# Kernel tuning notes

Hardware: AMD Instinct MI355X
Metric: run time of the kernel (lower is better)

## Reference

```python
import jax, jax.numpy as jnp
import numpy as np

N_NODES = 100000
N_EDGES = 1600000
IN_F = 512
OUT_F = 128


def setup_inputs() -> dict:
    key = jax.random.key(0)
    k1, k2, k3, k4, k5 = jax.random.split(key, 5)
    x = jax.random.normal(k1, (N_NODES, IN_F), dtype=jnp.float32)
    adj_row = jnp.sort(jax.random.randint(k2, (N_EDGES,), 0, N_NODES, dtype=jnp.int32))
    adj_col = jax.random.randint(k3, (N_EDGES,), 0, N_NODES, dtype=jnp.int32)
    adj_vals = jax.random.uniform(k4, (N_EDGES,), dtype=jnp.float32)
    # Xavier-uniform init like nn.init.xavier_uniform_
    limit = float(np.sqrt(6.0 / (IN_F + OUT_F)))
    weight = jax.random.uniform(k5, (IN_F, OUT_F), minval=-limit, maxval=limit, dtype=jnp.float32)
    return {"x": x, "adj_row": adj_row, "adj_col": adj_col, "adj_vals": adj_vals, "weight": weight}


def reference(x, adj_row, adj_col, adj_vals, weight):
    # support = input @ weight  (dense GEMM; torch.spmm with dense-equivalent input)
    support = x @ weight                      # [N, OUT_F]
    # output = adj @ support, adj in COO: gather cols, scale, segment-sum by row
    msgs = adj_vals[:, None] * support[adj_col]          # [E, OUT_F]
    output = jax.ops.segment_sum(msgs, adj_row, num_segments=N_NODES)  # [N, OUT_F]
    return output
```

## Files before the change

kernel.cpp:

```cpp
#include <hip/hip_runtime.h>
#include <hip/hip_bf16.h>

typedef __bf16 bf16;
typedef __attribute__((ext_vector_type(8))) __bf16 bf16x8;
typedef __attribute__((ext_vector_type(4))) __bf16 bf16x4;
typedef __attribute__((ext_vector_type(2))) __bf16 bf16x2;
typedef __attribute__((ext_vector_type(4))) float f32x4;

#define IN_F 512
#define OUT_F 128
#define BM 64
#define BK 64
#define NKT (IN_F / BK)
#define CHUNK 128
#define UNR 16

__global__ __launch_bounds__(256) void wt_convert_kernel(const float* __restrict__ w,
                                                         bf16* __restrict__ wt_frag) {
    int o = blockIdx.x * 256 + threadIdx.x;
    int e   = o & 7;
    int l   = (o >> 3) & 63;
    int nb  = (o >> 9) & 7;
    int kkt = o >> 12;
    int n = nb * 16 + (l & 15);
    int k = (kkt >> 1) * 64 + (kkt & 1) * 32 + (l >> 4) * 8 + e;
    wt_frag[o] = (bf16)w[k * OUT_F + n];
}

__global__ __launch_bounds__(256) void gemm_kernel(const float* __restrict__ x,
                                                   const bf16* __restrict__ wt_frag,
                                                   bf16* __restrict__ support,
                                                   float* __restrict__ out,
                                                   int n_nodes) {
    __shared__ bf16 As[2][BM * BK];

    const int tid  = threadIdx.x;
    const int lane = tid & 63;
    const int wid  = tid >> 6;
    const int row0 = blockIdx.x * BM;

    float4 av[4];

    auto load_tile = [&](int kt) {
        const int k0 = kt * BK;
        #pragma unroll
        for (int i = 0; i < 4; ++i) {
            int li = i * 256 + tid;
            int r = li >> 4, c4 = li & 15;
            int grow = row0 + r;
            float4 v = {0.f, 0.f, 0.f, 0.f};
            if (grow < n_nodes)
                v = *reinterpret_cast<const float4*>(x + (size_t)grow * IN_F + k0 + c4 * 4);
            av[i] = v;
        }
    };

    auto write_tile = [&](int buf) {
        char* Ab = (char*)As[buf];
        #pragma unroll
        for (int i = 0; i < 4; ++i) {
            int li = i * 256 + tid;
            int r = li >> 4, c4 = li & 15;
            bf16x4 b;
            b[0] = (bf16)av[i].x; b[1] = (bf16)av[i].y;
            b[2] = (bf16)av[i].z; b[3] = (bf16)av[i].w;
            *reinterpret_cast<bf16x4*>(Ab + ((r * 128 + c4 * 8) ^ ((r & 7) << 4))) = b;
        }
    };

    load_tile(0);

    {
        float4 z = {0.f, 0.f, 0.f, 0.f};
        const size_t lim = (size_t)n_nodes * OUT_F;
        #pragma unroll
        for (int i = 0; i < 8; ++i) {
            size_t off = (size_t)row0 * OUT_F + (size_t)(i * 256 + tid) * 4;
            if (off < lim)
                *reinterpret_cast<float4*>(out + off) = z;
        }
    }

    write_tile(0);
    __syncthreads();

    f32x4 acc[4][2] = {};

    for (int kt = 0; kt < NKT; ++kt) {
        const int cur = kt & 1;

        bf16x8 b[2][2];
        #pragma unroll
        for (int kk = 0; kk < 2; ++kk)
            #pragma unroll
            for (int n = 0; n < 2; ++n) {
                int f = (kt * 2 + kk) * 8 + (wid * 2 + n);
                b[kk][n] = *reinterpret_cast<const bf16x8*>(wt_frag + ((size_t)f * 64 + lane) * 8);
            }

        if (kt < NKT - 1) load_tile(kt + 1);

        const char* Ab = (const char*)As[cur];
        #pragma unroll
        for (int kk = 0; kk < 2; ++kk) {
            const int kbyte = kk * 64 + (lane >> 4) * 16;
            bf16x8 a[4];
            #pragma unroll
            for (int m = 0; m < 4; ++m) {
                int r = m * 16 + (lane & 15);
                a[m] = *reinterpret_cast<const bf16x8*>(Ab + ((r * 128 + kbyte) ^ ((r & 7) << 4)));
            }
            #pragma unroll
            for (int m = 0; m < 4; ++m)
                #pragma unroll
                for (int n = 0; n < 2; ++n)
                    acc[m][n] = __builtin_amdgcn_mfma_f32_16x16x32_bf16(a[m], b[kk][n], acc[m][n], 0, 0, 0);
        }

        if (kt < NKT - 1) {
            write_tile(cur ^ 1);
            __syncthreads();
        }
    }

    #pragma unroll
    for (int m = 0; m < 4; ++m) {
        #pragma unroll
        for (int n = 0; n < 2; ++n) {
            #pragma unroll
            for (int j = 0; j < 4; ++j) {
                int gm = row0 + m * 16 + (lane >> 4) * 4 + j;
                int gn = wid * 32 + n * 16 + (lane & 15);
                if (gm < n_nodes)
                    support[(size_t)gm * OUT_F + gn] = (bf16)acc[m][n][j];
            }
        }
    }
}

__global__ __launch_bounds__(64) void scatter_kernel(const int* __restrict__ adj_row,
                                                     const int* __restrict__ adj_col,
                                                     const float* __restrict__ adj_vals,
                                                     const bf16* __restrict__ support,
                                                     float* __restrict__ out,
                                                     int n_edges) {
    __shared__ int   srow[CHUNK];
    __shared__ int   scol[CHUNK];
    __shared__ float sval[CHUNK];

    const int t  = threadIdx.x;
    const int e0 = blockIdx.x * CHUNK;
    const int nE = min(CHUNK, n_edges - e0);

    for (int i = t; i < CHUNK; i += 64) {
        if (i < nE) {
            srow[i] = adj_row[e0 + i];
            scol[i] = adj_col[e0 + i];
            sval[i] = adj_vals[e0 + i];
        } else {
            srow[i] = adj_row[e0 + nE - 1];
            scol[i] = 0;
            sval[i] = 0.f;
        }
    }
    __syncthreads();

    const int firstRow = srow[0];

    float accx = 0.f, accy = 0.f;
    int   cur = firstRow;

    for (int i0 = 0; i0 < CHUNK; i0 += UNR) {
        float mx[UNR], my[UNR];
        #pragma unroll
        for (int u = 0; u < UNR; ++u) {
            int   c = scol[i0 + u];
            float s = sval[i0 + u];
            bf16x2 v = *reinterpret_cast<const bf16x2*>(support + (size_t)c * OUT_F + t * 2);
            mx[u] = s * (float)v[0];
            my[u] = s * (float)v[1];
        }
        #pragma unroll
        for (int u = 0; u < UNR; ++u) {
            int r = srow[i0 + u];
            if (r != cur) {
                float* dst = out + (size_t)cur * OUT_F + t * 2;
                if (cur == firstRow) {
                    atomicAdd(dst, accx); atomicAdd(dst + 1, accy);
                } else {
                    dst[0] = accx; dst[1] = accy;
                }
                accx = 0.f; accy = 0.f;
                cur = r;
            }
            accx += mx[u]; accy += my[u];
        }
    }
    float* dst = out + (size_t)cur * OUT_F + t * 2;
    atomicAdd(dst, accx); atomicAdd(dst + 1, accy);
}

extern "C" void kernel_launch(void* const* d_in, const int* in_sizes, int n_in,
                              void* d_out, int out_size, void* d_ws, size_t ws_size,
                              hipStream_t stream) {
    const float* x        = (const float*)d_in[0];
    const int*   adj_row  = (const int*)d_in[1];
    const int*   adj_col  = (const int*)d_in[2];
    const float* adj_vals = (const float*)d_in[3];
    const float* weight   = (const float*)d_in[4];
    float*       out      = (float*)d_out;

    const int n_nodes = in_sizes[0] / IN_F;
    const int n_edges = in_sizes[1];

    bf16* support = (bf16*)d_ws;
    bf16* wt_frag = (bf16*)((char*)d_ws + (size_t)n_nodes * OUT_F * 2);

    wt_convert_kernel<<<(IN_F * OUT_F) / 256, 256, 0, stream>>>(weight, wt_frag);

    int gemm_blocks = (n_nodes + BM - 1) / BM;
    gemm_kernel<<<gemm_blocks, 256, 0, stream>>>(x, wt_frag, support, out, n_nodes);

    int scat_blocks = (n_edges + CHUNK - 1) / CHUNK;
    scatter_kernel<<<scat_blocks, 64, 0, stream>>>(adj_row, adj_col, adj_vals,
                                                   support, out, n_edges);
}
```

Measured before the change: 126.3 us.

## Stage GEMM input tiles with direct global-to-LDS loads, converting to bf16 at read

The GEMM kernel now copies fp32 x tiles straight into shared memory with global_load_lds DMA, using an XOR-swizzled chunk layout. This replaces the old path that loaded into registers, converted to bf16 and wrote to LDS. The bf16 conversion now happens when A fragments are read from LDS before the MFMAs. The aim is to cut register pressure and VALU/LDS-write work in the load path and let loads overlap compute better. In exchange, LDS use doubles, every read converts fp32, and LDS read traffic per fragment doubles.

```diff
diff --git a/kernel.cpp b/kernel.cpp
--- a/kernel.cpp
+++ b/kernel.cpp
@@ -14,6 +14,12 @@
 #define NKT (IN_F / BK)
 #define CHUNK 128
 #define UNR 16
+
+__device__ __forceinline__ void gload_lds16(const void* g, void* l) {
+    __builtin_amdgcn_global_load_lds(
+        (const __attribute__((address_space(1))) void*)g,
+        (__attribute__((address_space(3))) void*)l, 16, 0, 0);
+}
 
 __global__ __launch_bounds__(256) void wt_convert_kernel(const float* __restrict__ w,
                                                          bf16* __restrict__ wt_frag) {
@@ -32,43 +38,29 @@
                                                    bf16* __restrict__ support,
                                                    float* __restrict__ out,
                                                    int n_nodes) {
-    __shared__ bf16 As[2][BM * BK];
+    __shared__ float As[2][BM * BK];
 
     const int tid  = threadIdx.x;
     const int lane = tid & 63;
     const int wid  = tid >> 6;
     const int row0 = blockIdx.x * BM;
 
-    float4 av[4];
-
-    auto load_tile = [&](int kt) {
+    auto stage_tile = [&](int kt, int buf) {
         const int k0 = kt * BK;
         #pragma unroll
         for (int i = 0; i < 4; ++i) {
-            int li = i * 256 + tid;
-            int r = li >> 4, c4 = li & 15;
+            int li  = i * 256 + tid;
+            int r   = li >> 4;
+            int c16 = li & 15;
             int grow = row0 + r;
-            float4 v = {0.f, 0.f, 0.f, 0.f};
-            if (grow < n_nodes)
-                v = *reinterpret_cast<const float4*>(x + (size_t)grow * IN_F + k0 + c4 * 4);
-            av[i] = v;
+            if (grow >= n_nodes) grow = n_nodes - 1;
+            const float* g = x + (size_t)grow * IN_F + k0 + ((c16 ^ (r & 7)) << 2);
+            float* l = &As[buf][(size_t)(i * 256 + (tid & ~63)) * 4];
+            gload_lds16(g, l);
         }
     };
 
-    auto write_tile = [&](int buf) {
-        char* Ab = (char*)As[buf];
-        #pragma unroll
-        for (int i = 0; i < 4; ++i) {
-            int li = i * 256 + tid;
-            int r = li >> 4, c4 = li & 15;
-            bf16x4 b;
-            b[0] = (bf16)av[i].x; b[1] = (bf16)av[i].y;
-            b[2] = (bf16)av[i].z; b[3] = (bf16)av[i].w;
-            *reinterpret_cast<bf16x4*>(Ab + ((r * 128 + c4 * 8) ^ ((r & 7) << 4))) = b;
-        }
-    };
-
-    load_tile(0);
+    stage_tile(0, 0);
 
     {
         float4 z = {0.f, 0.f, 0.f, 0.f};
@@ -80,8 +72,6 @@
                 *reinterpret_cast<float4*>(out + off) = z;
         }
     }
-
-    write_tile(0);
     __syncthreads();
 
     f32x4 acc[4][2] = {};
@@ -98,17 +88,22 @@
                 b[kk][n] = *reinterpret_cast<const bf16x8*>(wt_frag + ((size_t)f * 64 + lane) * 8);
             }
 
-        if (kt < NKT - 1) load_tile(kt + 1);
-
-        const char* Ab = (const char*)As[cur];
+        if (kt < NKT - 1) stage_tile(kt + 1, cur ^ 1);
+
+        const float* Af = As[cur];
         #pragma unroll
         for (int kk = 0; kk < 2; ++kk) {
-            const int kbyte = kk * 64 + (lane >> 4) * 16;
             bf16x8 a[4];
             #pragma unroll
             for (int m = 0; m < 4; ++m) {
-                int r = m * 16 + (lane & 15);
-                a[m] = *reinterpret_cast<const bf16x8*>(Ab + ((r * 128 + kbyte) ^ ((r & 7) << 4)));
+                int r  = m * 16 + (lane & 15);
+                int u0 = kk * 8 + (lane >> 4) * 2;
+                f32x4 f0 = *reinterpret_cast<const f32x4*>(Af + r * 64 + ((u0     ^ (r & 7)) << 2));
+                f32x4 f1 = *reinterpret_cast<const f32x4*>(Af + r * 64 + (((u0+1) ^ (r & 7)) << 2));
+                a[m][0] = (bf16)f0[0]; a[m][1] = (bf16)f0[1];
+                a[m][2] = (bf16)f0[2]; a[m][3] = (bf16)f0[3];
+                a[m][4] = (bf16)f1[0]; a[m][5] = (bf16)f1[1];
+                a[m][6] = (bf16)f1[2]; a[m][7] = (bf16)f1[3];
             }
             #pragma unroll
             for (int m = 0; m < 4; ++m)
@@ -117,10 +112,7 @@
                     acc[m][n] = __builtin_amdgcn_mfma_f32_16x16x32_bf16(a[m], b[kk][n], acc[m][n], 0, 0, 0);
         }
 
-        if (kt < NKT - 1) {
-            write_tile(cur ^ 1);
-            __syncthreads();
-        }
+        if (kt < NKT - 1) __syncthreads();
     }
 
     #pragma unroll
```

After: 129.0 us. +2.1%, slower.

## Build CSR row pointers and switch scatter to row-partitioned writes

Applied to the files above, without the earlier changes.

Adds a kernel that builds CSR row pointers from the sorted COO row array. The scatter kernel now gives each block a fixed range of rows and walks that row's edges in pages. Every output row is written exactly once with plain stores, and empty rows are zero-filled, so the atomics and the zeroing of the output inside the GEMM go away. In exchange there is an extra kernel launch, and work per block varies with row degree. Blocks are now 32 rows (about 512 edges) instead of 128 edges, so there are fewer blocks for parallelism.

```diff
diff --git a/kernel.cpp b/kernel.cpp
--- a/kernel.cpp
+++ b/kernel.cpp
@@ -12,7 +12,8 @@
 #define BM 64
 #define BK 64
 #define NKT (IN_F / BK)
-#define CHUNK 128
+#define RPB 32
+#define PAGE 512
 #define UNR 16
 
 __global__ __launch_bounds__(256) void wt_convert_kernel(const float* __restrict__ w,
@@ -27,10 +28,21 @@
     wt_frag[o] = (bf16)w[k * OUT_F + n];
 }
 
+__global__ __launch_bounds__(256) void row_ptr_kernel(const int* __restrict__ adj_row,
+                                                      int* __restrict__ row_ptr,
+                                                      int n_edges, int n_nodes) {
+    int e = blockIdx.x * 256 + threadIdx.x;
+    if (e >= n_edges) return;
+    int r1 = adj_row[e];
+    int r0 = (e == 0) ? -1 : adj_row[e - 1];
+    for (int r = r0 + 1; r <= r1; ++r) row_ptr[r] = e;
+    if (e == n_edges - 1)
+        for (int r = r1 + 1; r <= n_nodes; ++r) row_ptr[r] = n_edges;
+}
+
 __global__ __launch_bounds__(256) void gemm_kernel(const float* __restrict__ x,
                                                    const bf16* __restrict__ wt_frag,
                                                    bf16* __restrict__ support,
-                                                   float* __restrict__ out,
                                                    int n_nodes) {
     __shared__ bf16 As[2][BM * BK];
 
@@ -69,18 +81,6 @@
     };
 
     load_tile(0);
-
-    {
-        float4 z = {0.f, 0.f, 0.f, 0.f};
-        const size_t lim = (size_t)n_nodes * OUT_F;
-        #pragma unroll
-        for (int i = 0; i < 8; ++i) {
-            size_t off = (size_t)row0 * OUT_F + (size_t)(i * 256 + tid) * 4;
-            if (off < lim)
-                *reinterpret_cast<float4*>(out + off) = z;
-        }
-    }
-
     write_tile(0);
     __syncthreads();
 
@@ -142,62 +142,73 @@
                                                      const int* __restrict__ adj_col,
                                                      const float* __restrict__ adj_vals,
                                                      const bf16* __restrict__ support,
+                                                     const int* __restrict__ row_ptr,
                                                      float* __restrict__ out,
-                                                     int n_edges) {
-    __shared__ int   srow[CHUNK];
-    __shared__ int   scol[CHUNK];
-    __shared__ float sval[CHUNK];
-
-    const int t  = threadIdx.x;
-    const int e0 = blockIdx.x * CHUNK;
-    const int nE = min(CHUNK, n_edges - e0);
-
-    for (int i = t; i < CHUNK; i += 64) {
-        if (i < nE) {
-            srow[i] = adj_row[e0 + i];
-            scol[i] = adj_col[e0 + i];
-            sval[i] = adj_vals[e0 + i];
-        } else {
-            srow[i] = adj_row[e0 + nE - 1];
-            scol[i] = 0;
-            sval[i] = 0.f;
+                                                     int n_nodes) {
+    __shared__ int   srow[PAGE];
+    __shared__ int   scol[PAGE];
+    __shared__ float sval[PAGE];
+
+    const int t    = threadIdx.x;
+    const int r0   = blockIdx.x * RPB;
+    const int rEnd = min(r0 + RPB, n_nodes);
+    const int eLo  = row_ptr[r0];
+    const int eHi  = row_ptr[rEnd];
+
+    float accx = 0.f, accy = 0.f;
+    int   cur  = r0;
+
+    auto flush_to = [&](int rNew) {
+        if (cur < rEnd) {
+            float2 st = {accx, accy};
+            *reinterpret_cast<float2*>(out + (size_t)cur * OUT_F + t * 2) = st;
+        }
+        float2 z = {0.f, 0.f};
+        int zhi = rNew < rEnd ? rNew : rEnd;
+        for (int r = cur + 1; r < zhi; ++r)
+            *reinterpret_cast<float2*>(out + (size_t)r * OUT_F + t * 2) = z;
+        accx = 0.f; accy = 0.f;
+        cur = rNew;
+    };
+
+    for (int base = eLo; base < eHi; base += PAGE) {
+        const int nE = min(PAGE, eHi - base);
+        __syncthreads();
+        for (int i = t; i < nE; i += 64) {
+            srow[i] = adj_row[base + i];
+            scol[i] = adj_col[base + i];
+            sval[i] = adj_vals[base + i];
+        }
+        __syncthreads();
+        if (nE < PAGE) {
+            for (int i = nE + t; i < PAGE; i += 64) {
+                srow[i] = n_nodes;
+                scol[i] = 0;
+                sval[i] = 0.f;
+            }
+            __syncthreads();
+        }
+
+        for (int i0 = 0; i0 < PAGE; i0 += UNR) {
+            if (i0 >= nE) break;
+            float mx[UNR], my[UNR];
+            #pragma unroll
+            for (int u = 0; u < UNR; ++u) {
+                int   c = scol[i0 + u];
+                float s = sval[i0 + u];
+                bf16x2 v = *reinterpret_cast<const bf16x2*>(support + (size_t)c * OUT_F + t * 2);
+                mx[u] = s * (float)v[0];
+                my[u] = s * (float)v[1];
+            }
+            #pragma unroll
+            for (int u = 0; u < UNR; ++u) {
+                int r = srow[i0 + u];
+                if (r != cur) flush_to(r);
+                accx += mx[u]; accy += my[u];
+            }
         }
     }
-    __syncthreads();
-
-    const int firstRow = srow[0];
-
-    float accx = 0.f, accy = 0.f;
-    int   cur = firstRow;
-
-    for (int i0 = 0; i0 < CHUNK; i0 += UNR) {
-        float mx[UNR], my[UNR];
-        #pragma unroll
-        for (int u = 0; u < UNR; ++u) {
-            int   c = scol[i0 + u];
-            float s = sval[i0 + u];
-            bf16x2 v = *reinterpret_cast<const bf16x2*>(support + (size_t)c * OUT_F + t * 2);
-            mx[u] = s * (float)v[0];
-            my[u] = s * (float)v[1];
-        }
-        #pragma unroll
-        for (int u = 0; u < UNR; ++u) {
-            int r = srow[i0 + u];
-            if (r != cur) {
-                float* dst = out + (size_t)cur * OUT_F + t * 2;
-                if (cur == firstRow) {
-                    atomicAdd(dst, accx); atomicAdd(dst + 1, accy);
-                } else {
-                    dst[0] = accx; dst[1] = accy;
-                }
-                accx = 0.f; accy = 0.f;
-                cur = r;
-            }
-            accx += mx[u]; accy += my[u];
-        }
-    }
-    float* dst = out + (size_t)cur * OUT_F + t * 2;
-    atomicAdd(dst, accx); atomicAdd(dst + 1, accy);
+    flush_to(rEnd);
 }
 
 extern "C" void kernel_launch(void* const* d_in, const int* in_sizes, int n_in,
@@ -213,15 +224,20 @@
     const int n_nodes = in_sizes[0] / IN_F;
     const int n_edges = in_sizes[1];
 
-    bf16* support = (bf16*)d_ws;
-    bf16* wt_frag = (bf16*)((char*)d_ws + (size_t)n_nodes * OUT_F * 2);
+    char* ws = (char*)d_ws;
+    bf16* support = (bf16*)ws;
+    bf16* wt_frag = (bf16*)(ws + (size_t)n_nodes * OUT_F * 2);
+    int*  row_ptr = (int*)(ws + (size_t)n_nodes * OUT_F * 2 + IN_F * OUT_F * 2);
 
     wt_convert_kernel<<<(IN_F * OUT_F) / 256, 256, 0, stream>>>(weight, wt_frag);
 
+    row_ptr_kernel<<<(n_edges + 255) / 256, 256, 0, stream>>>(adj_row, row_ptr,
+                                                              n_edges, n_nodes);
+
     int gemm_blocks = (n_nodes + BM - 1) / BM;
-    gemm_kernel<<<gemm_blocks, 256, 0, stream>>>(x, wt_frag, support, out, n_nodes);
-
-    int scat_blocks = (n_edges + CHUNK - 1) / CHUNK;
+    gemm_kernel<<<gemm_blocks, 256, 0, stream>>>(x, wt_frag, support, n_nodes);
+
+    int scat_blocks = (n_nodes + RPB - 1) / RPB;
     scatter_kernel<<<scat_blocks, 64, 0, stream>>>(adj_row, adj_col, adj_vals,
-                                                   support, out, n_edges);
-}
+                                                   support, row_ptr, out, n_nodes);
+}
```

Result: faster. 123.4 us (-2.3%).
